# Kernel optimization log

Hardware: AMD Instinct MI355X
Metric: run time of the kernel (lower is better)

The kernel has to match this reference:

```python
import jax, jax.numpy as jnp
import numpy as np

B, S, L, D = 32, 8, 128, 768
A, T = 10, 8
VOCAB = 1000


def setup_inputs() -> dict:
    key = jax.random.key(0)
    k1, k2, k3, k4, k5 = jax.random.split(key, 5)
    sentence_ids = jax.random.randint(k1, (B, S, L), 0, VOCAB)
    sentence_attention_masks = jnp.ones((B, S, L), dtype=jnp.float32)
    # precomputed sum of last 4 BERT hidden layers (backbone excluded)
    sentence_embeddings = jax.random.normal(k2, (B, S, L, D), dtype=jnp.float32)
    predicate_ids = jax.random.randint(k3, (B, S, A, T), 0, VOCAB)
    arg0_ids = jax.random.randint(k4, (B, S, A, T), 0, VOCAB)
    arg1_ids = jax.random.randint(k5, (B, S, A, T), 0, VOCAB)
    return {
        "sentence_ids": sentence_ids,
        "sentence_attention_masks": sentence_attention_masks,
        "sentence_embeddings": sentence_embeddings,
        "predicate_ids": predicate_ids,
        "arg0_ids": arg0_ids,
        "arg1_ids": arg1_ids,
    }


def _mean_pool(emb, mask):
    # emb: [b,s,l,d], mask: [b,s,l] -> [b,s,d]
    masked_sum = jnp.einsum('bsld,bsl->bsd', emb, mask)
    counts = jnp.clip(mask.sum(-1, keepdims=True), 1, None)
    return masked_sum / counts


def _arg_embedding(arg_ids, sentence_ids, emb):
    # arg_ids: [b,s,a,t] int, sentence_ids: [b,s,l] int, emb: [b,s,l,d]
    # match[b,s,a,t,l] = sentence token l equals arg token t (and arg token != 0)
    match = (sentence_ids[:, :, None, None, :] == arg_ids[..., None]) & (arg_ids[..., None] != 0)
    mf = match.astype(emb.dtype)
    counts = mf.sum(-1)                                   # [b,s,a,t]
    summed = jnp.einsum('bsatl,bsld->bsatd', mf, emb)      # [b,s,a,t,d]
    avg = summed / jnp.maximum(counts, 1.0)[..., None]
    has = counts > 0                                       # [b,s,a,t]
    t_dim = arg_ids.shape[-1]
    # original loop overwrites per token -> keep the LAST token with a match
    last = (t_dim - 1) - jnp.argmax(has[..., ::-1], axis=-1)  # [b,s,a]
    sel = jnp.take_along_axis(avg, last[..., None, None], axis=3)[:, :, :, 0, :]
    valid = has.any(-1)                                    # [b,s,a]
    return jnp.where(valid[..., None], sel, jnp.zeros((), emb.dtype))


def reference(sentence_ids, sentence_attention_masks, sentence_embeddings,
              predicate_ids, arg0_ids, arg1_ids):
    sentence_embeddings_avg = _mean_pool(sentence_embeddings, sentence_attention_masks)
    predicate_embeddings = _arg_embedding(predicate_ids, sentence_ids, sentence_embeddings)
    arg0_embeddings = _arg_embedding(arg0_ids, sentence_ids, sentence_embeddings)
    arg1_embeddings = _arg_embedding(arg1_ids, sentence_ids, sentence_embeddings)
    return (sentence_embeddings_avg, predicate_embeddings, arg0_embeddings, arg1_embeddings)
```

## Files before the change

kernel.cpp:

```cpp
#include <hip/hip_runtime.h>

#define Bq 32
#define Sq 8
#define Lq 128
#define Dq 768
#define Aq 10
#define Tq 8

constexpr int D4    = Dq / 4;
constexpr int NPOOL = Bq * Sq * 4;
constexpr int NBSA  = Bq * Sq * Aq;
constexpr int NARG  = NBSA * 3;

__global__ __launch_bounds__(192) void srl_fused_k(
    const int* __restrict__ sids, const float* __restrict__ mask,
    const float* __restrict__ emb, const int* __restrict__ pred,
    const int* __restrict__ a0, const int* __restrict__ a1,
    float* __restrict__ out)
{
    int bid = blockIdx.x;
    int tid = threadIdx.x;

    if (bid < NPOOL) {
        int bs = bid >> 2;
        int q  = bid & 3;

        __shared__ float  marr[Lq];
        __shared__ float  msum;
        __shared__ float4 red[4][48];

        if (tid < Lq) marr[tid] = mask[(size_t)bs * Lq + tid];

        if (tid < 64) {
            float mv = mask[(size_t)bs * Lq + tid] +
                       mask[(size_t)bs * Lq + 64 + tid];
            for (int off = 32; off > 0; off >>= 1)
                mv += __shfl_xor(mv, off);
            if (tid == 0) msum = mv;
        }
        __syncthreads();

        int g = tid / 48;
        int c = tid - g * 48;

        const float4* eb = (const float4*)emb +
                           (size_t)bs * Lq * D4 + q * 48 + c;
        float4 acc = make_float4(0.f, 0.f, 0.f, 0.f);
#pragma unroll 8
        for (int l = 0; l < 32; ++l) {
            float  mv = marr[g * 32 + l];
            float4 v  = eb[(size_t)(g * 32 + l) * D4];
            acc.x += v.x * mv; acc.y += v.y * mv;
            acc.z += v.z * mv; acc.w += v.w * mv;
        }
        red[g][c] = acc;
        __syncthreads();

        if (tid < 48) {
            float4 a = red[0][tid], b = red[1][tid];
            float4 cc = red[2][tid], d = red[3][tid];
            float inv = 1.0f / fmaxf(msum, 1.0f);
            float4 r;
            r.x = (a.x + b.x + cc.x + d.x) * inv;
            r.y = (a.y + b.y + cc.y + d.y) * inv;
            r.z = (a.z + b.z + cc.z + d.z) * inv;
            r.w = (a.w + b.w + cc.w + d.w) * inv;
            ((float4*)out)[(size_t)bs * D4 + q * 48 + tid] = r;
        }
        return;
    }

    int j   = bid - NPOOL;
    int set = j / NBSA;
    int bsa = j - set * NBSA;
    int bs  = bsa / Aq;
    const int* ids = (set == 0) ? pred : ((set == 1) ? a0 : a1);

    int lane = tid & 63;
    int wv   = tid >> 6;

    __shared__ int sid[Lq];
    __shared__ int wcnt[3][Tq];
    __shared__ unsigned long long wb[3];
    __shared__ int mlist[Lq];

    if (tid < Lq) sid[tid] = sids[(size_t)bs * Lq + tid];

    int idreg[Tq];
#pragma unroll
    for (int t = 0; t < Tq; ++t) idreg[t] = ids[(size_t)bsa * Tq + t];
    __syncthreads();

    int myid = (tid < Lq) ? sid[tid] : -2;

#pragma unroll
    for (int t = 0; t < Tq; ++t) {
        bool m = (idreg[t] != 0) && (myid == idreg[t]);
        unsigned long long b = __ballot(m);
        if (lane == 0) wcnt[wv][t] = __popcll(b);
    }
    __syncthreads();

    int chosen = -1, ccount = 0;
#pragma unroll
    for (int t = Tq - 1; t >= 0; --t) {
        if (chosen == -1) {
            int cnt = wcnt[0][t] + wcnt[1][t] + wcnt[2][t];
            if (cnt > 0) { chosen = idreg[t]; ccount = cnt; }
        }
    }

    bool m = (myid == chosen);
    unsigned long long b = __ballot(m);
    if (lane == 0) wb[wv] = b;
    __syncthreads();
    int pos = (int)__popcll(b & ((1ull << lane) - 1ull));
    if (wv > 0) pos += (int)__popcll(wb[0]);
    if (wv > 1) pos += (int)__popcll(wb[1]);
    if (m) mlist[pos] = tid;
    __syncthreads();

    const float4* eb = (const float4*)emb + (size_t)bs * Lq * D4;
    float4 acc = make_float4(0.f, 0.f, 0.f, 0.f);
    for (int i = 0; i < ccount; ++i) {
        int l = mlist[i];
        float4 v = eb[(size_t)l * D4 + tid];
        acc.x += v.x; acc.y += v.y; acc.z += v.z; acc.w += v.w;
    }
    float inv = (ccount > 0) ? 1.0f / (float)ccount : 0.0f;
    float4 r = make_float4(acc.x * inv, acc.y * inv, acc.z * inv, acc.w * inv);

    float* outp = out + (size_t)Bq * Sq * Dq +
                  ((size_t)set * NBSA + bsa) * Dq;
    ((float4*)outp)[tid] = r;
}

extern "C" void kernel_launch(void* const* d_in, const int* in_sizes, int n_in,
                              void* d_out, int out_size, void* d_ws, size_t ws_size,
                              hipStream_t stream) {
    const int*   sids = (const int*)d_in[0];
    const float* mask = (const float*)d_in[1];
    const float* emb  = (const float*)d_in[2];
    const int*   pred = (const int*)d_in[3];
    const int*   a0   = (const int*)d_in[4];
    const int*   a1   = (const int*)d_in[5];
    float* out = (float*)d_out;

    srl_fused_k<<<NPOOL + NARG, 192, 0, stream>>>(sids, mask, emb,
                                                  pred, a0, a1, out);
}
```

Before: 27.66 us.

## Restructure work split: one block per sentence, wave-per-argument-set matching

Pool blocks now cover a whole sentence (all 128 tokens, 192 threads across D) instead of four blocks per sentence with a shared-memory reduction. Argument blocks drop from one per (b,s,a,set) to one per (b,s), with each wave handling one argument set and looping over the 10 arguments. Matching now uses wave-level shuffles and ballots with no shared memory or block syncs. This removes launch and sync overhead and lets each block reuse sentence ids across arguments. In exchange the grid shrinks from 8704 to 512 blocks, which lowers parallelism and memory-level concurrency and serialises the argument loop per wave.

```diff
diff --git a/kernel.cpp b/kernel.cpp
--- a/kernel.cpp
+++ b/kernel.cpp
@@ -8,9 +8,10 @@
 #define Tq 8
 
 constexpr int D4    = Dq / 4;
-constexpr int NPOOL = Bq * Sq * 4;
-constexpr int NBSA  = Bq * Sq * Aq;
-constexpr int NARG  = NBSA * 3;
+constexpr int NBS   = Bq * Sq;
+constexpr int NBSA  = NBS * Aq;
+constexpr int NPOOL = NBS;
+constexpr int NARG  = NBS;
 
 __global__ __launch_bounds__(192) void srl_fused_k(
     const int* __restrict__ sids, const float* __restrict__ mask,
@@ -22,15 +23,11 @@
     int tid = threadIdx.x;
 
     if (bid < NPOOL) {
-        int bs = bid >> 2;
-        int q  = bid & 3;
-
-        __shared__ float  marr[Lq];
-        __shared__ float  msum;
-        __shared__ float4 red[4][48];
+        int bs = bid;
+        __shared__ float marr[Lq];
+        __shared__ float msum;
 
         if (tid < Lq) marr[tid] = mask[(size_t)bs * Lq + tid];
-
         if (tid < 64) {
             float mv = mask[(size_t)bs * Lq + tid] +
                        mask[(size_t)bs * Lq + 64 + tid];
@@ -40,99 +37,81 @@
         }
         __syncthreads();
 
-        int g = tid / 48;
-        int c = tid - g * 48;
-
-        const float4* eb = (const float4*)emb +
-                           (size_t)bs * Lq * D4 + q * 48 + c;
+        const float4* eb = (const float4*)emb + (size_t)bs * Lq * D4 + tid;
         float4 acc = make_float4(0.f, 0.f, 0.f, 0.f);
-#pragma unroll 8
-        for (int l = 0; l < 32; ++l) {
-            float  mv = marr[g * 32 + l];
-            float4 v  = eb[(size_t)(g * 32 + l) * D4];
+#pragma unroll 16
+        for (int l = 0; l < Lq; ++l) {
+            float  mv = marr[l];
+            float4 v  = eb[(size_t)l * D4];
             acc.x += v.x * mv; acc.y += v.y * mv;
             acc.z += v.z * mv; acc.w += v.w * mv;
         }
-        red[g][c] = acc;
-        __syncthreads();
-
-        if (tid < 48) {
-            float4 a = red[0][tid], b = red[1][tid];
-            float4 cc = red[2][tid], d = red[3][tid];
-            float inv = 1.0f / fmaxf(msum, 1.0f);
-            float4 r;
-            r.x = (a.x + b.x + cc.x + d.x) * inv;
-            r.y = (a.y + b.y + cc.y + d.y) * inv;
-            r.z = (a.z + b.z + cc.z + d.z) * inv;
-            r.w = (a.w + b.w + cc.w + d.w) * inv;
-            ((float4*)out)[(size_t)bs * D4 + q * 48 + tid] = r;
-        }
+        float inv = 1.0f / fmaxf(msum, 1.0f);
+        float4 r = make_float4(acc.x * inv, acc.y * inv,
+                               acc.z * inv, acc.w * inv);
+        ((float4*)out)[(size_t)bs * D4 + tid] = r;
         return;
     }
 
-    int j   = bid - NPOOL;
-    int set = j / NBSA;
-    int bsa = j - set * NBSA;
-    int bs  = bsa / Aq;
+    int bs   = bid - NPOOL;
+    int set  = tid >> 6;
+    int lane = tid & 63;
     const int* ids = (set == 0) ? pred : ((set == 1) ? a0 : a1);
 
-    int lane = tid & 63;
-    int wv   = tid >> 6;
-
-    __shared__ int sid[Lq];
-    __shared__ int wcnt[3][Tq];
-    __shared__ unsigned long long wb[3];
-    __shared__ int mlist[Lq];
-
-    if (tid < Lq) sid[tid] = sids[(size_t)bs * Lq + tid];
-
-    int idreg[Tq];
-#pragma unroll
-    for (int t = 0; t < Tq; ++t) idreg[t] = ids[(size_t)bsa * Tq + t];
-    __syncthreads();
-
-    int myid = (tid < Lq) ? sid[tid] : -2;
-
-#pragma unroll
-    for (int t = 0; t < Tq; ++t) {
-        bool m = (idreg[t] != 0) && (myid == idreg[t]);
-        unsigned long long b = __ballot(m);
-        if (lane == 0) wcnt[wv][t] = __popcll(b);
-    }
-    __syncthreads();
-
-    int chosen = -1, ccount = 0;
-#pragma unroll
-    for (int t = Tq - 1; t >= 0; --t) {
-        if (chosen == -1) {
-            int cnt = wcnt[0][t] + wcnt[1][t] + wcnt[2][t];
-            if (cnt > 0) { chosen = idreg[t]; ccount = cnt; }
-        }
-    }
-
-    bool m = (myid == chosen);
-    unsigned long long b = __ballot(m);
-    if (lane == 0) wb[wv] = b;
-    __syncthreads();
-    int pos = (int)__popcll(b & ((1ull << lane) - 1ull));
-    if (wv > 0) pos += (int)__popcll(wb[0]);
-    if (wv > 1) pos += (int)__popcll(wb[1]);
-    if (m) mlist[pos] = tid;
-    __syncthreads();
+    int s0 = sids[(size_t)bs * Lq + lane];
+    int s1 = sids[(size_t)bs * Lq + 64 + lane];
 
     const float4* eb = (const float4*)emb + (size_t)bs * Lq * D4;
-    float4 acc = make_float4(0.f, 0.f, 0.f, 0.f);
-    for (int i = 0; i < ccount; ++i) {
-        int l = mlist[i];
-        float4 v = eb[(size_t)l * D4 + tid];
-        acc.x += v.x; acc.y += v.y; acc.z += v.z; acc.w += v.w;
+
+    for (int a = 0; a < Aq; ++a) {
+        int bsa = bs * Aq + a;
+        int idv = (lane < Tq) ? ids[(size_t)bsa * Tq + lane] : 0;
+
+        unsigned long long B0 = 0, B1 = 0;
+        int ccount = 0;
+#pragma unroll
+        for (int t = Tq - 1; t >= 0; --t) {
+            if (ccount == 0) {
+                int idt = __shfl(idv, t);
+                if (idt != 0) {
+                    unsigned long long b0 = __ballot(s0 == idt);
+                    unsigned long long b1 = __ballot(s1 == idt);
+                    int c = (int)(__popcll(b0) + __popcll(b1));
+                    if (c > 0) { B0 = b0; B1 = b1; ccount = c; }
+                }
+            }
+        }
+
+        float4 acc0 = make_float4(0.f, 0.f, 0.f, 0.f);
+        float4 acc1 = acc0, acc2 = acc0;
+        unsigned long long b = B0;
+        while (b) {
+            int l = (int)__builtin_ctzll(b); b &= b - 1;
+            float4 v0 = eb[(size_t)l * D4 + lane];
+            float4 v1 = eb[(size_t)l * D4 + 64 + lane];
+            float4 v2 = eb[(size_t)l * D4 + 128 + lane];
+            acc0.x += v0.x; acc0.y += v0.y; acc0.z += v0.z; acc0.w += v0.w;
+            acc1.x += v1.x; acc1.y += v1.y; acc1.z += v1.z; acc1.w += v1.w;
+            acc2.x += v2.x; acc2.y += v2.y; acc2.z += v2.z; acc2.w += v2.w;
+        }
+        b = B1;
+        while (b) {
+            int l = (int)__builtin_ctzll(b) + 64; b &= b - 1;
+            float4 v0 = eb[(size_t)l * D4 + lane];
+            float4 v1 = eb[(size_t)l * D4 + 64 + lane];
+            float4 v2 = eb[(size_t)l * D4 + 128 + lane];
+            acc0.x += v0.x; acc0.y += v0.y; acc0.z += v0.z; acc0.w += v0.w;
+            acc1.x += v1.x; acc1.y += v1.y; acc1.z += v1.z; acc1.w += v1.w;
+            acc2.x += v2.x; acc2.y += v2.y; acc2.z += v2.z; acc2.w += v2.w;
+        }
+
+        float inv = (ccount > 0) ? 1.0f / (float)ccount : 0.0f;
+        float4* o4 = (float4*)out +
+                     ((size_t)NBS + (size_t)set * NBSA + bsa) * D4;
+        o4[lane]       = make_float4(acc0.x*inv, acc0.y*inv, acc0.z*inv, acc0.w*inv);
+        o4[64 + lane]  = make_float4(acc1.x*inv, acc1.y*inv, acc1.z*inv, acc1.w*inv);
+        o4[128 + lane] = make_float4(acc2.x*inv, acc2.y*inv, acc2.z*inv, acc2.w*inv);
     }
-    float inv = (ccount > 0) ? 1.0f / (float)ccount : 0.0f;
-    float4 r = make_float4(acc.x * inv, acc.y * inv, acc.z * inv, acc.w * inv);
-
-    float* outp = out + (size_t)Bq * Sq * Dq +
-                  ((size_t)set * NBSA + bsa) * Dq;
-    ((float4*)outp)[tid] = r;
 }
 
 extern "C" void kernel_launch(void* const* d_in, const int* in_sizes, int n_in,
```

After: 25.96 us. 1.07x faster.
